# Kernel tuning notes

Measured on AMD Instinct MI355X. Metric: run time of the kernel, lower is better.

Reference implementation:

```python
import jax, jax.numpy as jnp
import numpy as np

B, N, DIM = 16, 1024, 768
H = 12
HD = DIM // H
SCALE = HD ** -0.5

def setup_inputs() -> dict:
    key = jax.random.key(0)
    k1, k2, k3, k4 = jax.random.split(key, 4)
    x = jax.random.normal(k1, (B, N, DIM), dtype=jnp.float32)
    # qkv: Linear(dim, 3*dim, bias=False); torch weight is [out, in]
    w_qkv = jax.random.normal(k2, (3 * DIM, DIM), dtype=jnp.float32) * (DIM ** -0.5)
    # proj: Linear(dim, dim) with bias
    w_proj = jax.random.normal(k3, (DIM, DIM), dtype=jnp.float32) * (DIM ** -0.5)
    b_proj = jax.random.normal(k4, (DIM,), dtype=jnp.float32) * 0.02
    return {"x": x, "w_qkv": w_qkv, "w_proj": w_proj, "b_proj": b_proj}

def reference(x, w_qkv, w_proj, b_proj):
    B_, N_, D_ = x.shape
    # qkv projection: [B, N, 3*D] -> [3, B, H, N, HD]
    qkv = jnp.einsum('bnd,ed->bne', x, w_qkv)
    qkv = qkv.reshape(B_, N_, 3, H, HD).transpose(2, 0, 3, 1, 4)
    q, k, v = qkv[0], qkv[1], qkv[2]
    # attention scores [B, H, N, N]
    attn = jnp.einsum('bhqd,bhkd->bhqk', q, k) * SCALE
    attn = jax.nn.softmax(attn, axis=-1)
    # weighted values -> [B, N, D]
    out = jnp.einsum('bhqk,bhkd->bhqd', attn, v)
    out = out.transpose(0, 2, 1, 3).reshape(B_, N_, D_)
    # output projection
    out = jnp.einsum('bnd,ed->bne', out, w_proj) + b_proj
    return out
```

## Files before the change

### kernel.cpp

```cpp
#include <hip/hip_runtime.h>
#include <cstdint>

#define B_SZ 16
#define SEQ 1024
#define DIM 768
#define NH 12
#define HD 64
#define M_TOTAL (B_SZ*SEQ)
#define QKV_OUT (3*DIM)
#define EXP2_SCALE 0.18033688011f

typedef _Float16 f16;
typedef __attribute__((ext_vector_type(8))) f16 f16x8;
typedef __attribute__((ext_vector_type(4))) f16 f16x4;
typedef __attribute__((ext_vector_type(2))) __fp16 pk16x2;
typedef __attribute__((ext_vector_type(4))) short s4_t;
typedef __attribute__((ext_vector_type(4))) float f32x4;
typedef unsigned int u32;
typedef const __attribute__((address_space(1))) u32* gas_t;
typedef __attribute__((address_space(3))) u32* las_t;

union U4 { pk16x2 h2[2]; f16x4 v; };
union U8 { pk16x2 h2[4]; f16x8 v; };
union HS { f16 h; short s; };

__device__ __forceinline__ void async16(const void* g, void* l) {
    __builtin_amdgcn_global_load_lds((gas_t)g, (las_t)l, 16, 0, 0);
}
__device__ __forceinline__ f32x4 mfma32h(f16x8 a, f16x8 b, f32x4 c) {
    return __builtin_amdgcn_mfma_f32_16x16x32_f16(a, b, c, 0, 0, 0);
}
__device__ __forceinline__ f16x8 ldfragh(const short* p) {
    return *(const f16x8*)p;
}

__global__ void cvt_kernel(const float* __restrict__ x, const float* __restrict__ wq,
                           const float* __restrict__ wp,
                           short* __restrict__ xb, short* __restrict__ wqb, short* __restrict__ wpb) {
    const long nx = (long)M_TOTAL * DIM / 4;
    const long nq = (long)QKV_OUT * DIM / 4;
    const long np = (long)DIM * DIM / 4;
    const long total = nx + nq + np;
    for (long i = (long)blockIdx.x * blockDim.x + threadIdx.x; i < total;
         i += (long)gridDim.x * blockDim.x) {
        const float4* src; short* dst; long off;
        if (i < nx)            { src = (const float4*)x;  dst = xb;  off = i; }
        else if (i < nx + nq)  { src = (const float4*)wq; dst = wqb; off = i - nx; }
        else                   { src = (const float4*)wp; dst = wpb; off = i - nx - nq; }
        float4 v = src[off];
        U4 u;
        u.h2[0] = __builtin_amdgcn_cvt_pkrtz(v.x, v.y);
        u.h2[1] = __builtin_amdgcn_cvt_pkrtz(v.z, v.w);
        *(f16x4*)(dst + off * 4) = u.v;
    }
}

template<int EPI, int N, int K>
__global__ __launch_bounds__(256) void gemm_bt(const short* __restrict__ A,
                                               const short* __restrict__ Bm,
                                               short* __restrict__ Cq, short* __restrict__ Ck,
                                               short* __restrict__ Cv,
                                               float* __restrict__ Cout,
                                               const float* __restrict__ bias) {
    __shared__ short As[128 * 32];
    __shared__ short Bs[128 * 32];
    const int tid = threadIdx.x;
    const int w = tid >> 6, l = tid & 63, quad = l >> 4, l15 = l & 15;
    const int wr = w >> 1, wc = w & 1;
    const int m0 = blockIdx.y * 128, n0 = blockIdx.x * 128;

    f32x4 acc[4][4];
#pragma unroll
    for (int i = 0; i < 4; ++i)
#pragma unroll
        for (int j = 0; j < 4; ++j) acc[i][j] = (f32x4){0.f, 0.f, 0.f, 0.f};

    for (int kt = 0; kt < K / 32; ++kt) {
#pragma unroll
        for (int i = 0; i < 2; ++i) {
            int c = i * 256 + tid;
            int row = c >> 2, kc = c & 3;
            async16(&A[(size_t)(m0 + row) * K + kt * 32 + kc * 8], &As[c * 8]);
            async16(&Bm[(size_t)(n0 + row) * K + kt * 32 + kc * 8], &Bs[c * 8]);
        }
        __syncthreads();
        f16x8 af[4], bf[4];
#pragma unroll
        for (int rt = 0; rt < 4; ++rt)
            af[rt] = ldfragh(&As[(wr * 64 + rt * 16 + l15) * 32 + quad * 8]);
#pragma unroll
        for (int ct = 0; ct < 4; ++ct)
            bf[ct] = ldfragh(&Bs[(wc * 64 + ct * 16 + l15) * 32 + quad * 8]);
#pragma unroll
        for (int rt = 0; rt < 4; ++rt)
#pragma unroll
            for (int ct = 0; ct < 4; ++ct)
                acc[rt][ct] = mfma32h(af[rt], bf[ct], acc[rt][ct]);
        __syncthreads();
    }

#pragma unroll
    for (int rt = 0; rt < 4; ++rt) {
#pragma unroll
        for (int ct = 0; ct < 4; ++ct) {
            int col = n0 + wc * 64 + ct * 16 + l15;
            if (EPI == 0) {
                int s = col / DIM;
                int h = (col - s * DIM) >> 6, hd = col & 63;
                int mbase = m0 + wr * 64 + rt * 16 + quad * 4;
                int b = mbase >> 10, nn = mbase & 1023;
                if (s == 2) {
                    U4 u;
                    u.h2[0] = __builtin_amdgcn_cvt_pkrtz(acc[rt][ct][0], acc[rt][ct][1]);
                    u.h2[1] = __builtin_amdgcn_cvt_pkrtz(acc[rt][ct][2], acc[rt][ct][3]);
                    *(f16x4*)&Cv[(((size_t)b * NH + h) * HD + hd) * SEQ + nn] = u.v;
                } else {
                    short* dst = (s == 0) ? Cq : Ck;
                    const float qs = (s == 0) ? EXP2_SCALE : 1.0f;
#pragma unroll
                    for (int r = 0; r < 4; ++r) {
                        HS t; t.h = (f16)(acc[rt][ct][r] * qs);
                        dst[(((size_t)b * NH + h) * SEQ + nn + r) * HD + hd] = t.s;
                    }
                }
            } else {
                float bv = bias[col];
#pragma unroll
                for (int r = 0; r < 4; ++r) {
                    int m = m0 + wr * 64 + rt * 16 + quad * 4 + r;
                    Cout[(size_t)m * N + col] = acc[rt][ct][r] + bv;
                }
            }
        }
    }
}

__global__ __launch_bounds__(256) void attn_kernel(const short* __restrict__ Q,
                                                   const short* __restrict__ Km,
                                                   const short* __restrict__ Vt,
                                                   short* __restrict__ O) {
    __shared__ short lds[4][4096];
    const int tid = threadIdx.x;
    const int w = tid >> 6, l = tid & 63, quad = l >> 4, l15 = l & 15;
    const int bid = blockIdx.x;
    const int xcd = bid & 7, kk = bid >> 3;
    const int head = xcd + 8 * (kk >> 3);
    const int q0 = (kk & 7) * 128 + w * 32;
    const int b = head / NH, h = head - b * NH;
    const short* Qp = Q + (size_t)head * (SEQ * HD);
    const short* Kp = Km + (size_t)head * (SEQ * HD);
    const short* Vp = Vt + (size_t)head * (SEQ * HD);

    f16x8 qf[2][2];
#pragma unroll
    for (int qt = 0; qt < 2; ++qt)
#pragma unroll
        for (int hf = 0; hf < 2; ++hf)
            qf[qt][hf] = *(const f16x8*)&Qp[(q0 + qt * 16 + l15) * HD + hf * 32 + quad * 8];

    f32x4 oacc[2][4];
#pragma unroll
    for (int qt = 0; qt < 2; ++qt)
#pragma unroll
        for (int ht = 0; ht < 4; ++ht) oacc[qt][ht] = (f32x4){0.f, 0.f, 0.f, 0.f};
    float psum[2] = {0.f, 0.f};

    const int kr = tid >> 3, kc = tid & 7;
    const int kcc = kc ^ ((kr & 3) ^ (((kr >> 3) & 3) << 1));
    const short* kSrc = Kp + kr * HD + kcc * 8;
    const int kDst = kr * 64 + kc * 8;
    const int vr = tid >> 2, vc = tid & 3;
    const int vcc = vc ^ ((vr >> 1) & 3);
    const short* vSrc = Vp + vr * SEQ + vcc * 8;
    const int vDst = 2048 + vr * 32 + vc * 8;

#define STAGE(bf, g) do {                                   \
        async16(kSrc + (g) * (32 * HD), &lds[bf][kDst]);    \
        async16(vSrc + (g) * 32, &lds[bf][vDst]);           \
    } while (0)

    const int rA = 8 * (l15 >> 2) + (l15 & 3);
    const int sk = (l15 & 3) ^ ((l15 >> 2) << 1);
    const int offK = rA * 64 + ((quad ^ sk) * 8);
    const int offV = 2048 + l15 * 32 + ((quad ^ ((l15 >> 1) & 3)) * 8);

    STAGE(0, 0); STAGE(1, 1); STAGE(2, 2);

    for (int g = 0; g < 32; ++g) {
        if (g <= 29)      asm volatile("s_waitcnt vmcnt(4)" ::: "memory");
        else if (g == 30) asm volatile("s_waitcnt vmcnt(2)" ::: "memory");
        else              asm volatile("s_waitcnt vmcnt(0)" ::: "memory");
        __builtin_amdgcn_s_barrier();
        if (g < 29) STAGE((g + 3) & 3, g + 3);

        const short* kb = &lds[g & 3][0];
        f16x8 kA0 = ldfragh(kb + offK);
        f16x8 kA1 = ldfragh(kb + (offK ^ 32));
        f16x8 kB0 = ldfragh(kb + offK + 256);
        f16x8 kB1 = ldfragh(kb + (offK ^ 32) + 256);
        f16x8 v0 = ldfragh(kb + offV);
        f16x8 v1 = ldfragh(kb + offV + 512);
        f16x8 v2 = ldfragh(kb + offV + 1024);
        f16x8 v3 = ldfragh(kb + offV + 1536);

        __builtin_amdgcn_s_setprio(1);
#pragma unroll
        for (int qt = 0; qt < 2; ++qt) {
            f32x4 sA = (f32x4){0.f, 0.f, 0.f, 0.f};
            sA = mfma32h(kA0, qf[qt][0], sA);
            sA = mfma32h(kA1, qf[qt][1], sA);
            f32x4 sB = (f32x4){0.f, 0.f, 0.f, 0.f};
            sB = mfma32h(kB0, qf[qt][0], sB);
            sB = mfma32h(kB1, qf[qt][1], sB);
            float eA0 = __builtin_amdgcn_exp2f(sA[0]);
            float eA1 = __builtin_amdgcn_exp2f(sA[1]);
            float eA2 = __builtin_amdgcn_exp2f(sA[2]);
            float eA3 = __builtin_amdgcn_exp2f(sA[3]);
            float eB0 = __builtin_amdgcn_exp2f(sB[0]);
            float eB1 = __builtin_amdgcn_exp2f(sB[1]);
            float eB2 = __builtin_amdgcn_exp2f(sB[2]);
            float eB3 = __builtin_amdgcn_exp2f(sB[3]);
            psum[qt] += ((eA0 + eA1) + (eA2 + eA3)) + ((eB0 + eB1) + (eB2 + eB3));
            U8 u;
            u.h2[0] = __builtin_amdgcn_cvt_pkrtz(eA0, eA1);
            u.h2[1] = __builtin_amdgcn_cvt_pkrtz(eA2, eA3);
            u.h2[2] = __builtin_amdgcn_cvt_pkrtz(eB0, eB1);
            u.h2[3] = __builtin_amdgcn_cvt_pkrtz(eB2, eB3);
            oacc[qt][0] = mfma32h(v0, u.v, oacc[qt][0]);
            oacc[qt][1] = mfma32h(v1, u.v, oacc[qt][1]);
            oacc[qt][2] = mfma32h(v2, u.v, oacc[qt][2]);
            oacc[qt][3] = mfma32h(v3, u.v, oacc[qt][3]);
        }
        __builtin_amdgcn_s_setprio(0);
    }
#undef STAGE

#pragma unroll
    for (int qt = 0; qt < 2; ++qt) {
        psum[qt] += __shfl_xor(psum[qt], 16);
        psum[qt] += __shfl_xor(psum[qt], 32);
    }

#pragma unroll
    for (int qt = 0; qt < 2; ++qt) {
        float rinv = 1.0f / psum[qt];
        short* orow = &O[((size_t)b * SEQ + q0 + qt * 16 + l15) * DIM + h * HD + quad * 4];
#pragma unroll
        for (int ht = 0; ht < 4; ++ht) {
            U4 u;
            u.h2[0] = __builtin_amdgcn_cvt_pkrtz(oacc[qt][ht][0] * rinv, oacc[qt][ht][1] * rinv);
            u.h2[1] = __builtin_amdgcn_cvt_pkrtz(oacc[qt][ht][2] * rinv, oacc[qt][ht][3] * rinv);
            *(f16x4*)(orow + ht * 16) = u.v;
        }
    }
}

extern "C" void kernel_launch(void* const* d_in, const int* in_sizes, int n_in,
                              void* d_out, int out_size, void* d_ws, size_t ws_size,
                              hipStream_t stream) {
    const float* x      = (const float*)d_in[0];
    const float* w_qkv  = (const float*)d_in[1];
    const float* w_proj = (const float*)d_in[2];
    const float* b_proj = (const float*)d_in[3];
    float* out = (float*)d_out;

    short* p = (short*)d_ws;
    short* Xb  = p; p += (size_t)M_TOTAL * DIM;
    short* Wqb = p; p += (size_t)QKV_OUT * DIM;
    short* Wpb = p; p += (size_t)DIM * DIM;
    short* Qb  = p; p += (size_t)B_SZ * NH * SEQ * HD;
    short* Kb  = p; p += (size_t)B_SZ * NH * SEQ * HD;
    short* Vtb = p; p += (size_t)B_SZ * NH * SEQ * HD;
    short* Ob  = p; p += (size_t)M_TOTAL * DIM;

    cvt_kernel<<<1024, 256, 0, stream>>>(x, w_qkv, w_proj, Xb, Wqb, Wpb);
    gemm_bt<0, QKV_OUT, DIM><<<dim3(QKV_OUT / 128, M_TOTAL / 128), 256, 0, stream>>>(
        Xb, Wqb, Qb, Kb, Vtb, nullptr, nullptr);
    attn_kernel<<<B_SZ * NH * (SEQ / 128), 256, 0, stream>>>(Qb, Kb, Vtb, Ob);
    gemm_bt<1, DIM, DIM><<<dim3(DIM / 128, M_TOTAL / 128), 256, 0, stream>>>(
        Ob, Wpb, nullptr, nullptr, nullptr, out, b_proj);
}
```

Baseline: 293.1 us.

## Rewrite GEMM as 256x256 tile, 8-wave, double-buffered LDS pipeline with swizzle

The projection GEMMs move from 128x128 tiles with 4 waves and a synchronous single-buffer K loop to 256x256 tiles with 8 waves. K tiles of 64 are double-buffered in 128KB of LDS, with staged async loads interleaved with MFMA quads behind barriers and vmcnt waits. LDS columns are XOR-swizzled to avoid bank conflicts, MFMA sections run at raised priority, and block IDs are remapped across XCDs. The aim is to hide global-load latency and raise arithmetic intensity, at the cost of heavy register and LDS use (one block per CU) and fewer blocks for the small output projection (192 blocks).

```diff
diff --git a/kernel.cpp b/kernel.cpp
--- a/kernel.cpp
+++ b/kernel.cpp
@@ -55,60 +55,153 @@
     }
 }
 
+template<int QM, int QN>
+__device__ __forceinline__ void mfma_quad(f32x4 (&acc)[8][4], const f16x8 (&af)[4][2],
+                                          const f16x8 (&bf)[4][2]) {
+#pragma unroll
+    for (int r = 0; r < 4; ++r)
+#pragma unroll
+        for (int c = 0; c < 2; ++c) {
+            f32x4 t = acc[QM * 4 + r][QN * 2 + c];
+            t = mfma32h(af[r][0], bf[QN * 2 + c][0], t);
+            t = mfma32h(af[r][1], bf[QN * 2 + c][1], t);
+            acc[QM * 4 + r][QN * 2 + c] = t;
+        }
+}
+
 template<int EPI, int N, int K>
-__global__ __launch_bounds__(256) void gemm_bt(const short* __restrict__ A,
-                                               const short* __restrict__ Bm,
-                                               short* __restrict__ Cq, short* __restrict__ Ck,
-                                               short* __restrict__ Cv,
-                                               float* __restrict__ Cout,
-                                               const float* __restrict__ bias) {
-    __shared__ short As[128 * 32];
-    __shared__ short Bs[128 * 32];
+__global__ __launch_bounds__(512, 2) void gemm_bt(const short* __restrict__ A,
+                                                  const short* __restrict__ Bm,
+                                                  short* __restrict__ Cq, short* __restrict__ Ck,
+                                                  short* __restrict__ Cv,
+                                                  float* __restrict__ Cout,
+                                                  const float* __restrict__ bias) {
+    static_assert(K % 128 == 0, "even K-tile count required");
+    constexpr int NT = K / 64;
+    constexpr int NIT = NT / 2;
+    __shared__ short lds[65536];
+
     const int tid = threadIdx.x;
-    const int w = tid >> 6, l = tid & 63, quad = l >> 4, l15 = l & 15;
-    const int wr = w >> 1, wc = w & 1;
-    const int m0 = blockIdx.y * 128, n0 = blockIdx.x * 128;
-
-    f32x4 acc[4][4];
-#pragma unroll
-    for (int i = 0; i < 4; ++i)
+    const int l = tid & 63, quad = l >> 4, l15 = l & 15, l7 = l15 & 7;
+    const int w = tid >> 6, wr = w >> 2, wc = w & 3;
+
+    const int gx = gridDim.x;
+    const int nwg = gx * (int)gridDim.y;
+    int fid = (int)blockIdx.y * gx + (int)blockIdx.x;
+    fid = (fid & 7) * (nwg >> 3) + (fid >> 3);
+    const int m0 = (fid / gx) * 256;
+    const int n0 = (fid % gx) * 256;
+
+    const int srow = tid >> 3, sc = tid & 7;
+    const int scc = sc ^ (srow & 7);
+    const short* Asrc = A + (size_t)(m0 + srow) * K + scc * 8;
+    const short* Bsrc = Bm + (size_t)(n0 + srow) * K + scc * 8;
+    const int sdst = srow * 64 + sc * 8;
+
+#define STAGE_A(t, hi) do {                                              \
+        const int sb_ = ((t) & 1) * 32768 + (hi) * 8192;                 \
+        const size_t go_ = (size_t)((hi) * 128) * K + (size_t)(t) * 64;  \
+        async16(Asrc + go_, &lds[sb_ + sdst]);                           \
+        async16(Asrc + go_ + (size_t)64 * K, &lds[sb_ + sdst + 4096]);   \
+    } while (0)
+#define STAGE_B(t, hi) do {                                              \
+        const int sb_ = ((t) & 1) * 32768 + 16384 + (hi) * 8192;         \
+        const size_t go_ = (size_t)((hi) * 128) * K + (size_t)(t) * 64;  \
+        async16(Bsrc + go_, &lds[sb_ + sdst]);                           \
+        async16(Bsrc + go_ + (size_t)64 * K, &lds[sb_ + sdst + 4096]);   \
+    } while (0)
+
+    const int aoff = wr * 8192 + l15 * 64;
+    const int boff = 16384 + wc * 4096 + l15 * 64;
+    const int c0 = (quad ^ l7) * 8;
+    const int c1 = ((4 + quad) ^ l7) * 8;
+
+#define RD_A(SB, MHALF) do {                                                                  \
+        const int ab_ = (SB) + aoff + (MHALF) * 4096;                                         \
+        af[0][0] = ldfragh(&lds[ab_ + c0]);        af[0][1] = ldfragh(&lds[ab_ + c1]);        \
+        af[1][0] = ldfragh(&lds[ab_ + 1024 + c0]); af[1][1] = ldfragh(&lds[ab_ + 1024 + c1]); \
+        af[2][0] = ldfragh(&lds[ab_ + 2048 + c0]); af[2][1] = ldfragh(&lds[ab_ + 2048 + c1]); \
+        af[3][0] = ldfragh(&lds[ab_ + 3072 + c0]); af[3][1] = ldfragh(&lds[ab_ + 3072 + c1]); \
+    } while (0)
+#define RD_B(SB, NHALF) do {                                                                             \
+        const int bb_ = (SB) + boff + (NHALF) * 2048;                                                    \
+        bf[(NHALF)*2][0]   = ldfragh(&lds[bb_ + c0]);        bf[(NHALF)*2][1]   = ldfragh(&lds[bb_ + c1]);        \
+        bf[(NHALF)*2+1][0] = ldfragh(&lds[bb_ + 1024 + c0]); bf[(NHALF)*2+1][1] = ldfragh(&lds[bb_ + 1024 + c1]); \
+    } while (0)
+
+#define BAR1() __builtin_amdgcn_s_barrier()
+#define BAR2() do { __builtin_amdgcn_s_barrier(); __builtin_amdgcn_sched_barrier(0); } while (0)
+#define VMC4() asm volatile("s_waitcnt vmcnt(4)" ::: "memory")
+#define VMC0() asm volatile("s_waitcnt vmcnt(0)" ::: "memory")
+#define MQ(QM, QN) do {                                        \
+        __builtin_amdgcn_s_setprio(1);                         \
+        mfma_quad<QM, QN>(acc, af, bf);                        \
+        __builtin_amdgcn_s_setprio(0);                         \
+    } while (0)
+
+    f32x4 acc[8][4];
+#pragma unroll
+    for (int i = 0; i < 8; ++i)
 #pragma unroll
         for (int j = 0; j < 4; ++j) acc[i][j] = (f32x4){0.f, 0.f, 0.f, 0.f};
-
-    for (int kt = 0; kt < K / 32; ++kt) {
-#pragma unroll
-        for (int i = 0; i < 2; ++i) {
-            int c = i * 256 + tid;
-            int row = c >> 2, kc = c & 3;
-            async16(&A[(size_t)(m0 + row) * K + kt * 32 + kc * 8], &As[c * 8]);
-            async16(&Bm[(size_t)(n0 + row) * K + kt * 32 + kc * 8], &Bs[c * 8]);
-        }
-        __syncthreads();
-        f16x8 af[4], bf[4];
-#pragma unroll
-        for (int rt = 0; rt < 4; ++rt)
-            af[rt] = ldfragh(&As[(wr * 64 + rt * 16 + l15) * 32 + quad * 8]);
-#pragma unroll
-        for (int ct = 0; ct < 4; ++ct)
-            bf[ct] = ldfragh(&Bs[(wc * 64 + ct * 16 + l15) * 32 + quad * 8]);
-#pragma unroll
-        for (int rt = 0; rt < 4; ++rt)
-#pragma unroll
-            for (int ct = 0; ct < 4; ++ct)
-                acc[rt][ct] = mfma32h(af[rt], bf[ct], acc[rt][ct]);
-        __syncthreads();
-    }
-
-#pragma unroll
-    for (int rt = 0; rt < 4; ++rt) {
+    f16x8 af[4][2], bf[4][2];
+
+    STAGE_B(0, 0); STAGE_B(0, 1); STAGE_A(0, 0); STAGE_A(0, 1);
+    STAGE_B(1, 0); STAGE_B(1, 1);
+    VMC4();
+    BAR2();
+
+    for (int i = 0; i < NIT; ++i) {
+        const int to = 2 * i + 1, t2 = 2 * i + 2, t3 = 2 * i + 3;
+        RD_A(0, 0); RD_B(0, 0);
+        STAGE_A(to, 0);
+        BAR1(); MQ(0, 0); BAR2();
+
+        RD_B(0, 1);
+        STAGE_A(to, 1);
+        BAR1(); MQ(0, 1); BAR2();
+
+        RD_A(0, 1);
+        if (t2 < NT) STAGE_B(t2, 0);
+        BAR1(); MQ(1, 0); BAR2();
+
+        if (t2 < NT) STAGE_B(t2, 1);
+        BAR1(); MQ(1, 1);
+        if (i == NIT - 1) VMC0(); else VMC4();
+        BAR2();
+
+        RD_A(32768, 0); RD_B(32768, 0);
+        if (t2 < NT) STAGE_A(t2, 0);
+        BAR1(); MQ(0, 0); BAR2();
+
+        RD_B(32768, 1);
+        if (t2 < NT) STAGE_A(t2, 1);
+        BAR1(); MQ(0, 1); BAR2();
+
+        RD_A(32768, 1);
+        if (t3 < NT) STAGE_B(t3, 0);
+        BAR1(); MQ(1, 0); BAR2();
+
+        if (t3 < NT) STAGE_B(t3, 1);
+        BAR1(); MQ(1, 1);
+        if (i == NIT - 1) VMC0(); else VMC4();
+        BAR2();
+    }
+#undef STAGE_A
+#undef STAGE_B
+#undef RD_A
+#undef RD_B
+
+#pragma unroll
+    for (int rt = 0; rt < 8; ++rt) {
+        const int mrow = m0 + wr * 128 + (rt >> 2) * 64 + (rt & 3) * 16 + quad * 4;
 #pragma unroll
         for (int ct = 0; ct < 4; ++ct) {
-            int col = n0 + wc * 64 + ct * 16 + l15;
+            const int col = n0 + wc * 64 + (ct >> 1) * 32 + (ct & 1) * 16 + l15;
             if (EPI == 0) {
                 int s = col / DIM;
                 int h = (col - s * DIM) >> 6, hd = col & 63;
-                int mbase = m0 + wr * 64 + rt * 16 + quad * 4;
-                int b = mbase >> 10, nn = mbase & 1023;
+                int b = mrow >> 10, nn = mrow & 1023;
                 if (s == 2) {
                     U4 u;
                     u.h2[0] = __builtin_amdgcn_cvt_pkrtz(acc[rt][ct][0], acc[rt][ct][1]);
@@ -126,10 +219,8 @@
             } else {
                 float bv = bias[col];
 #pragma unroll
-                for (int r = 0; r < 4; ++r) {
-                    int m = m0 + wr * 64 + rt * 16 + quad * 4 + r;
-                    Cout[(size_t)m * N + col] = acc[rt][ct][r] + bv;
-                }
+                for (int r = 0; r < 4; ++r)
+                    Cout[(size_t)(mrow + r) * N + col] = acc[rt][ct][r] + bv;
             }
         }
     }
@@ -274,9 +365,9 @@
     short* Ob  = p; p += (size_t)M_TOTAL * DIM;
 
     cvt_kernel<<<1024, 256, 0, stream>>>(x, w_qkv, w_proj, Xb, Wqb, Wpb);
-    gemm_bt<0, QKV_OUT, DIM><<<dim3(QKV_OUT / 128, M_TOTAL / 128), 256, 0, stream>>>(
+    gemm_bt<0, QKV_OUT, DIM><<<dim3(QKV_OUT / 256, M_TOTAL / 256), 512, 0, stream>>>(
         Xb, Wqb, Qb, Kb, Vtb, nullptr, nullptr);
     attn_kernel<<<B_SZ * NH * (SEQ / 128), 256, 0, stream>>>(Qb, Kb, Vtb, Ob);
-    gemm_bt<1, DIM, DIM><<<dim3(DIM / 128, M_TOTAL / 128), 256, 0, stream>>>(
+    gemm_bt<1, DIM, DIM><<<dim3(DIM / 256, M_TOTAL / 256), 512, 0, stream>>>(
         Ob, Wpb, nullptr, nullptr, nullptr, out, b_proj);
 }
```

Result: faster. 273.6 us (-6.7%).
